# Kernel optimization log

Measured on AMD Instinct MI355X. Metric: run time of the kernel, lower is better.

## Reference

```python
import jax, jax.numpy as jnp
import numpy as np

DIM_X, DIM_Y, DIM_D, DIM_H = 100, 1, 100, 256
T = 1.0


def setup_inputs() -> dict:
    key = jax.random.key(0)
    ks = jax.random.split(key, 10)
    B, N = 2048, 128

    def lin(k, fi, fo):
        # kaiming-ish scaling so the relu MLP stays well-conditioned
        return (jax.random.normal(k, (fi, fo), jnp.float32) / np.sqrt(fi)).astype(jnp.float32)

    return {
        "W_noise": jax.random.normal(ks[0], (B, DIM_D, N), jnp.float32),  # unscaled randn; *sqrt(dt) in reference
        "signs": jax.random.randint(ks[1], (N,), 0, 2).astype(jnp.int32),  # 0/1 -> mapped to +-1
        "x0": jnp.ones((DIM_X,), jnp.float32),
        "y0": jax.random.uniform(ks[2], (DIM_Y,), jnp.float32),
        "Wi": lin(ks[3], DIM_X + 1, DIM_H),
        "bi": jnp.zeros((DIM_H,), jnp.float32),
        "Wh1": lin(ks[4], DIM_H, DIM_H),
        "bh1": jnp.zeros((DIM_H,), jnp.float32),
        "Wh2": lin(ks[5], DIM_H, DIM_H),
        "bh2": jnp.zeros((DIM_H,), jnp.float32),
        "Wo": lin(ks[6], DIM_H, DIM_Y * DIM_D),
        "bo": jnp.zeros((DIM_Y * DIM_D,), jnp.float32),
        "batch_size": B,
        "N": N,
    }


def reference(W_noise, signs, x0, y0, Wi, bi, Wh1, bh1, Wh2, bh2, Wo, bo, batch_size, N):
    dt = jnp.float32(T / N)
    sqdt = jnp.sqrt(dt)
    sqrt2 = jnp.sqrt(jnp.float32(2.0))
    B = W_noise.shape[0]

    W = W_noise * sqdt                                   # Brownian increments [B, D, N]
    s_pm = (2 * signs - 1).astype(jnp.float32)           # +-1 per step
    ones_col = jnp.ones((B, 1), jnp.float32)

    def phi(u):  # relu MLP -> [B, dim_y, dim_d]
        h = jax.nn.relu(u @ Wi + bi)
        h = jax.nn.relu(h @ Wh1 + bh1)
        h = jax.nn.relu(h @ Wh2 + bh2)
        return (h @ Wo + bo).reshape(-1, DIM_Y, DIM_D)

    def f_fn(t, x, y, z):  # driver f(t,x,y,z) = ||z||^2 over d
        return jnp.sum(z * z, axis=-1)  # [B, dim_y]

    x_init = x0 + jnp.zeros((B, DIM_X), jnp.float32)
    y_init = y0 + jnp.zeros((B, DIM_Y), jnp.float32)

    xs = (jnp.moveaxis(W, 2, 0), s_pm, jnp.arange(N, dtype=jnp.float32))

    def step(carry, inp):
        x, y = carry
        w, s, i = inp                      # w: [B, D]
        t0 = dt * i
        t1 = dt * (i + 1.0)
        sdt = s * sqdt
        z = phi(jnp.concatenate([x, ones_col * t0], axis=1))
        # b = 0, sigma = sqrt(2)*I  =>  matmul(sigma, w -+ S*sqrt(dt)) = sqrt(2)*(w -+ sdt)
        k1 = sqrt2 * (w - sdt)
        k2 = sqrt2 * (w + sdt)
        y1 = -f_fn(t0, x, y, z) * dt + jnp.einsum('byd,bd->by', z, w - sdt)
        z_new = phi(jnp.concatenate([x + k1, ones_col * t1], axis=1))
        y2 = -f_fn(t1, x, y + y1, z) * dt + jnp.einsum('byd,bd->by', z_new, w + sdt)
        return (x + 0.5 * (k1 + k2), y + 0.5 * (y1 + y2)), None

    (x, y), _ = jax.lax.scan(step, (x_init, y_init), xs)
    return x, y
```

## Files before the change

kernel.cpp:

```cpp
#include <hip/hip_runtime.h>
#include <hip/hip_bf16.h>

typedef __hip_bfloat16 bf16;
typedef __attribute__((ext_vector_type(8)))  short bf16x8v;
typedef __attribute__((ext_vector_type(16))) float f32x16;
typedef __attribute__((ext_vector_type(4)))  short short4v;

#define B_SZ   2048
#define NSTEP  128
#define DD     100
#define DX     100
#define DH     256

__device__ __constant__ const float DT_   = 0.0078125f;
__device__ __constant__ const float SQDT_ = 0.08838834764831845f;
__device__ __constant__ const float C1_   = 0.125f;

__global__ __launch_bounds__(256) void pack_kernel(
    const float* __restrict__ Wi, const float* __restrict__ Wh1,
    const float* __restrict__ Wh2, const float* __restrict__ Wo,
    const float* __restrict__ bi, const float* __restrict__ bh1,
    const float* __restrict__ bh2, const float* __restrict__ bo,
    bf16* __restrict__ wfWi, bf16* __restrict__ wfWh1,
    bf16* __restrict__ wfWh2, bf16* __restrict__ wfWo,
    float* __restrict__ biases)
{
    const int bid = blockIdx.x;
    const float* W; bf16* dst; int Kact, Nact, NTILE, total, base;
    if (bid < 112)      { W = Wi;  dst = wfWi;  Kact = 101; Nact = 256; NTILE = 8; total = 28672; base = 0;   }
    else if (bid < 368) { W = Wh1; dst = wfWh1; Kact = 256; Nact = 256; NTILE = 8; total = 65536; base = 112; }
    else if (bid < 624) { W = Wh2; dst = wfWh2; Kact = 256; Nact = 256; NTILE = 8; total = 65536; base = 368; }
    else if (bid < 752) { W = Wo;  dst = wfWo;  Kact = 256; Nact = 100; NTILE = 4; total = 32768; base = 624; }
    else {
        int i = (bid - 752) * 256 + threadIdx.x;
        if (i < 256) biases[i] = bi[i];
        else if (i < 512) biases[i] = bh1[i - 256];
        else if (i < 768) biases[i] = bh2[i - 512];
        else if (i < 896) biases[i] = (i - 768 < DD) ? bo[i - 768] : 0.f;
        return;
    }
    int idx = (bid - base) * 256 + threadIdx.x;
    if (idx >= total) return;
    int j = idx & 7;
    int l = (idx >> 3) & 63;
    int frag = idx >> 9;
    int t = frag % NTILE;
    int c = frag / NTILE;
    int n = t * 32 + (l & 31);
    int k = c * 16 + (l >> 5) * 8 + j;
    float v = (k < Kact && n < Nact) ? W[(size_t)k * Nact + n] : 0.f;
    dst[idx] = __float2bfloat16(v);
}

__global__ __launch_bounds__(128) void xprep_kernel(
    const float* __restrict__ Wn, const float* __restrict__ x0,
    float* __restrict__ xckpt, float* __restrict__ xout)
{
    __shared__ float w_l[DD * 129];
    const int b = blockIdx.x, tid = threadIdx.x;
    const float* wb = Wn + (size_t)b * DD * NSTEP;

    for (int idx = tid; idx < DD * NSTEP; idx += 128) {
        int d = idx >> 7, i = idx & 127;
        w_l[d * 129 + i] = wb[idx];
    }
    __syncthreads();

    if (tid < DD) {
        float x = x0[tid];
#pragma unroll 1
        for (int i = 0; i < NSTEP; ++i) {
            if ((i & 31) == 0)
                xckpt[((size_t)b * 4 + (i >> 5)) * DX + tid] = x;
            x += C1_ * w_l[tid * 129 + i];
        }
        xout[(size_t)b * DX + tid] = x;
    }
}

template<int KC, int NTT, int NT, bool RELU>
__device__ __forceinline__ void layer32(
    char* __restrict__ buf,
    const bf16* __restrict__ wfrag, const float* __restrict__ bias,
    int lane, int t0)
{
    const int mrow = lane & 31;
    const int kg   = lane >> 5;
    const int ma = mrow, mb = 32 + mrow;
    const int sa = (ma & 15) << 4, sb = (mb & 15) << 4;

    f32x16 acc[NT][2];
#pragma unroll
    for (int t = 0; t < NT; ++t)
#pragma unroll
        for (int mt = 0; mt < 2; ++mt)
#pragma unroll
            for (int e = 0; e < 16; ++e) acc[t][mt][e] = 0.f;

    const char* wptr = (const char*)wfrag + (size_t)t0 * 1024 + (size_t)lane * 16;

    bf16x8v bc0 = *(const bf16x8v*)(buf + ma * 512 + ((kg * 16) ^ sa));
    bf16x8v bc1 = *(const bf16x8v*)(buf + mb * 512 + ((kg * 16) ^ sb));
    bf16x8v ac[NT];
#pragma unroll
    for (int t = 0; t < NT; ++t)
        ac[t] = *(const bf16x8v*)(wptr + (size_t)t * 1024);

#pragma unroll
    for (int c = 0; c < KC; ++c) {
        const int cn = (c + 1 < KC) ? c + 1 : c;
        const int ncol = cn * 32 + kg * 16;
        bf16x8v bn0 = *(const bf16x8v*)(buf + ma * 512 + (ncol ^ sa));
        bf16x8v bn1 = *(const bf16x8v*)(buf + mb * 512 + (ncol ^ sb));
        bf16x8v an[NT];
#pragma unroll
        for (int t = 0; t < NT; ++t)
            an[t] = *(const bf16x8v*)(wptr + (size_t)(cn * NTT + t) * 1024);

        __builtin_amdgcn_s_setprio(1);
#pragma unroll
        for (int t = 0; t < NT; ++t) {
            acc[t][0] = __builtin_amdgcn_mfma_f32_32x32x16_bf16(ac[t], bc0, acc[t][0], 0, 0, 0);
            acc[t][1] = __builtin_amdgcn_mfma_f32_32x32x16_bf16(ac[t], bc1, acc[t][1], 0, 0, 0);
        }
        __builtin_amdgcn_s_setprio(0);

        bc0 = bn0; bc1 = bn1;
#pragma unroll
        for (int t = 0; t < NT; ++t) ac[t] = an[t];
    }

    __syncthreads();

#pragma unroll
    for (int t = 0; t < NT; ++t) {
#pragma unroll
        for (int g = 0; g < 4; ++g) {
            const int nb = (t0 + t) * 32 + g * 8 + kg * 4;
            const float4 bv = *(const float4*)(bias + nb);
#pragma unroll
            for (int mt = 0; mt < 2; ++mt) {
                const int m = mt * 32 + mrow;
                float v0 = acc[t][mt][g * 4 + 0] + bv.x;
                float v1 = acc[t][mt][g * 4 + 1] + bv.y;
                float v2 = acc[t][mt][g * 4 + 2] + bv.z;
                float v3 = acc[t][mt][g * 4 + 3] + bv.w;
                if (RELU) {
                    v0 = fmaxf(v0, 0.f); v1 = fmaxf(v1, 0.f);
                    v2 = fmaxf(v2, 0.f); v3 = fmaxf(v3, 0.f);
                }
                bf16 h0 = __float2bfloat16(v0), h1 = __float2bfloat16(v1);
                bf16 h2 = __float2bfloat16(v2), h3 = __float2bfloat16(v3);
                short4v pv;
                pv[0] = *(short*)&h0; pv[1] = *(short*)&h1;
                pv[2] = *(short*)&h2; pv[3] = *(short*)&h3;
                *(short4v*)(buf + m * 512 + ((nb * 2) ^ ((m & 15) << 4))) = pv;
            }
        }
    }
}

__global__ __launch_bounds__(256, 3) void mlp_kernel(
    const float* __restrict__ Wn, const int* __restrict__ signs,
    const float* __restrict__ xckpt,
    const bf16* __restrict__ wfWi, const bf16* __restrict__ wfWh1,
    const bf16* __restrict__ wfWh2, const bf16* __restrict__ wfWo,
    const float* __restrict__ biases, float* __restrict__ incr)
{
    __shared__ char  buf[64 * 512];
    __shared__ float noise[DD * 33];
    __shared__ float s_l32[32];
    __shared__ float Sz2[64], Szw[64];
    const int tid = threadIdx.x;
    const int lane = tid & 63, w = tid >> 6;
    const int b = blockIdx.x >> 2, ch = blockIdx.x & 3;
    const int i0 = ch * 32;
    const size_t row0 = (size_t)blockIdx.x * 64;
    const float* wnb = Wn + (size_t)b * DD * NSTEP;

    for (int idx = tid; idx < DD * 32; idx += 256) {
        int d = idx >> 5, j = idx & 31;
        noise[d * 33 + j] = wnb[d * NSTEP + i0 + j];
    }
    if (tid < 32) s_l32[tid] = 2.f * (float)signs[i0 + tid] - 1.f;
    __syncthreads();

    if (tid < DD) {
        const int d = tid;
        float x = xckpt[((size_t)b * 4 + ch) * DX + d];
#pragma unroll 1
        for (int j = 0; j < 32; ++j) {
            float wn = noise[d * 33 + j];
            float s  = s_l32[j];
            int r0 = j * 2;
            bf16 h0 = __float2bfloat16(x);
            bf16 h1 = __float2bfloat16(x + C1_ * (wn - s));
            *(short*)(buf + r0 * 512 + ((d * 2) ^ ((r0 & 15) << 4))) = *(short*)&h0;
            *(short*)(buf + (r0 + 1) * 512 + ((d * 2) ^ (((r0 + 1) & 15) << 4))) = *(short*)&h1;
            x += C1_ * wn;
        }
    } else if (tid < 164) {
        const int r = tid - 100;
        const int i = i0 + (r >> 1), h = r & 1;
        bf16 tv = __float2bfloat16(DT_ * (float)(i + h));
        char* rb = buf + r * 512;
        const int sw = (r & 15) << 4;
        *(short*)(rb + (200 ^ sw)) = *(short*)&tv;
        *(short*)(rb + (202 ^ sw)) = 0;
        *(short*)(rb + (204 ^ sw)) = 0;
        *(short*)(rb + (206 ^ sw)) = 0;
        *(uint4*)(rb + (208 ^ sw)) = (uint4){0, 0, 0, 0};
    }
    __syncthreads();

    layer32<7,  8, 2, true >(buf, wfWi,  biases,        lane, w * 2);
    __syncthreads();
    layer32<16, 8, 2, true >(buf, wfWh1, biases + 256,  lane, w * 2);
    __syncthreads();
    layer32<16, 8, 2, true >(buf, wfWh2, biases + 512,  lane, w * 2);
    __syncthreads();
    layer32<16, 4, 1, false>(buf, wfWo,  biases + 768,  lane, w);
    __syncthreads();

    {
        const int r = tid >> 2, q = tid & 3;
        const int jj = r >> 1, h = r & 1;
        const float s = s_l32[jj];
        const float sdt = s * SQDT_;
        float sz2 = 0.f, szw = 0.f;
        for (int d = q; d < DD; d += 4) {
            unsigned short zb = *(const unsigned short*)(buf + r * 512 + ((d * 2) ^ ((r & 15) << 4)));
            union { unsigned int u; float f; } cv; cv.u = ((unsigned int)zb) << 16;
            float z = cv.f;
            float wv = SQDT_ * noise[d * 33 + jj];
            float wt = h ? (wv + sdt) : (wv - sdt);
            sz2 += z * z;
            szw += z * wt;
        }
        sz2 += __shfl_xor(sz2, 1); sz2 += __shfl_xor(sz2, 2);
        szw += __shfl_xor(szw, 1); szw += __shfl_xor(szw, 2);
        if (q == 0) { Sz2[r] = sz2; Szw[r] = szw; }
    }
    __syncthreads();

    if (tid < 32) {
        int rr = tid * 2;
        incr[row0 / 2 + tid] = -Sz2[rr] * DT_ + 0.5f * (Szw[rr] + Szw[rr + 1]);
    }
}

__global__ __launch_bounds__(128) void y_kernel(
    const float* __restrict__ incr, const float* __restrict__ y0,
    float* __restrict__ yout)
{
    const int b = blockIdx.x, tid = threadIdx.x;
    float v = incr[(size_t)b * NSTEP + tid];
#pragma unroll
    for (int off = 1; off < 64; off <<= 1) v += __shfl_xor(v, off);
    __shared__ float partial[2];
    if ((tid & 63) == 0) partial[tid >> 6] = v;
    __syncthreads();
    if (tid == 0) yout[b] = y0[0] + partial[0] + partial[1];
}

extern "C" void kernel_launch(void* const* d_in, const int* in_sizes, int n_in,
                              void* d_out, int out_size, void* d_ws, size_t ws_size,
                              hipStream_t stream) {
    (void)in_sizes; (void)n_in; (void)out_size; (void)ws_size;
    const float* Wn    = (const float*)d_in[0];
    const int*   signs = (const int*)d_in[1];
    const float* x0    = (const float*)d_in[2];
    const float* y0    = (const float*)d_in[3];
    const float* Wi    = (const float*)d_in[4];
    const float* bi    = (const float*)d_in[5];
    const float* Wh1   = (const float*)d_in[6];
    const float* bh1   = (const float*)d_in[7];
    const float* Wh2   = (const float*)d_in[8];
    const float* bh2   = (const float*)d_in[9];
    const float* Wo    = (const float*)d_in[10];
    const float* bo    = (const float*)d_in[11];

    float* out  = (float*)d_out;
    float* xout = out;
    float* yout = out + (size_t)B_SZ * DX;

    char* ws = (char*)d_ws;
    size_t off = 0;
    bf16*  wfWi   = (bf16*)(ws + off); off += 28672 * sizeof(bf16);
    bf16*  wfWh1  = (bf16*)(ws + off); off += 65536 * sizeof(bf16);
    bf16*  wfWh2  = (bf16*)(ws + off); off += 65536 * sizeof(bf16);
    bf16*  wfWo   = (bf16*)(ws + off); off += 32768 * sizeof(bf16);
    float* biases = (float*)(ws + off); off += 896 * sizeof(float);
    float* xckpt  = (float*)(ws + off); off += (size_t)B_SZ * 4 * DX * sizeof(float);
    float* incr   = (float*)(ws + off); off += (size_t)B_SZ * NSTEP * sizeof(float);

    pack_kernel<<<756, 256, 0, stream>>>(Wi, Wh1, Wh2, Wo, bi, bh1, bh2, bo,
                                         wfWi, wfWh1, wfWh2, wfWo, biases);
    xprep_kernel<<<B_SZ, 128, 0, stream>>>(Wn, x0, xckpt, xout);
    mlp_kernel<<<B_SZ * 4, 256, 0, stream>>>(Wn, signs, xckpt,
                                             wfWi, wfWh1, wfWh2, wfWo, biases, incr);
    y_kernel<<<B_SZ, 128, 0, stream>>>(incr, y0, yout);
}
```

Measured before the change: 276.7 us.

## Double MLP block to 512 threads with one N-tile per wave

The MLP kernel now launches 512 threads (8 waves) per block instead of 256. In the hidden layers each wave owns a single 32-column output tile instead of two. In the output layer the waves split both the N tiles and the two 32-row M halves. The aim is more waves per block to hide LDS and weight-load latency and to spread the MFMA work more finely, at the cost of fewer accumulators per wave, more barrier participants and idle threads in the scalar sections.

```diff
diff --git a/kernel.cpp b/kernel.cpp
--- a/kernel.cpp
+++ b/kernel.cpp
@@ -78,89 +78,82 @@
     }
 }
 
-template<int KC, int NTT, int NT, bool RELU>
-__device__ __forceinline__ void layer32(
+template<int KC, int NTT, int MT, bool RELU>
+__device__ __forceinline__ void layer32w(
     char* __restrict__ buf,
     const bf16* __restrict__ wfrag, const float* __restrict__ bias,
-    int lane, int t0)
+    int lane, int t0, int m0)
 {
     const int mrow = lane & 31;
     const int kg   = lane >> 5;
-    const int ma = mrow, mb = 32 + mrow;
-    const int sa = (ma & 15) << 4, sb = (mb & 15) << 4;
-
-    f32x16 acc[NT][2];
-#pragma unroll
-    for (int t = 0; t < NT; ++t)
-#pragma unroll
-        for (int mt = 0; mt < 2; ++mt)
-#pragma unroll
-            for (int e = 0; e < 16; ++e) acc[t][mt][e] = 0.f;
+
+    f32x16 acc[MT];
+#pragma unroll
+    for (int mt = 0; mt < MT; ++mt)
+#pragma unroll
+        for (int e = 0; e < 16; ++e) acc[mt][e] = 0.f;
 
     const char* wptr = (const char*)wfrag + (size_t)t0 * 1024 + (size_t)lane * 16;
 
-    bf16x8v bc0 = *(const bf16x8v*)(buf + ma * 512 + ((kg * 16) ^ sa));
-    bf16x8v bc1 = *(const bf16x8v*)(buf + mb * 512 + ((kg * 16) ^ sb));
-    bf16x8v ac[NT];
-#pragma unroll
-    for (int t = 0; t < NT; ++t)
-        ac[t] = *(const bf16x8v*)(wptr + (size_t)t * 1024);
+    bf16x8v bc[MT];
+#pragma unroll
+    for (int mt = 0; mt < MT; ++mt) {
+        const int m = m0 + mt * 32 + mrow;
+        bc[mt] = *(const bf16x8v*)(buf + m * 512 + ((kg * 16) ^ ((m & 15) << 4)));
+    }
+    bf16x8v ac = *(const bf16x8v*)(wptr);
 
 #pragma unroll
     for (int c = 0; c < KC; ++c) {
         const int cn = (c + 1 < KC) ? c + 1 : c;
         const int ncol = cn * 32 + kg * 16;
-        bf16x8v bn0 = *(const bf16x8v*)(buf + ma * 512 + (ncol ^ sa));
-        bf16x8v bn1 = *(const bf16x8v*)(buf + mb * 512 + (ncol ^ sb));
-        bf16x8v an[NT];
-#pragma unroll
-        for (int t = 0; t < NT; ++t)
-            an[t] = *(const bf16x8v*)(wptr + (size_t)(cn * NTT + t) * 1024);
+        bf16x8v bn[MT];
+#pragma unroll
+        for (int mt = 0; mt < MT; ++mt) {
+            const int m = m0 + mt * 32 + mrow;
+            bn[mt] = *(const bf16x8v*)(buf + m * 512 + (ncol ^ ((m & 15) << 4)));
+        }
+        bf16x8v an = *(const bf16x8v*)(wptr + (size_t)(cn * NTT) * 1024);
 
         __builtin_amdgcn_s_setprio(1);
 #pragma unroll
-        for (int t = 0; t < NT; ++t) {
-            acc[t][0] = __builtin_amdgcn_mfma_f32_32x32x16_bf16(ac[t], bc0, acc[t][0], 0, 0, 0);
-            acc[t][1] = __builtin_amdgcn_mfma_f32_32x32x16_bf16(ac[t], bc1, acc[t][1], 0, 0, 0);
-        }
+        for (int mt = 0; mt < MT; ++mt)
+            acc[mt] = __builtin_amdgcn_mfma_f32_32x32x16_bf16(ac, bc[mt], acc[mt], 0, 0, 0);
         __builtin_amdgcn_s_setprio(0);
 
-        bc0 = bn0; bc1 = bn1;
-#pragma unroll
-        for (int t = 0; t < NT; ++t) ac[t] = an[t];
-    }
-
-    __syncthreads();
-
-#pragma unroll
-    for (int t = 0; t < NT; ++t) {
-#pragma unroll
-        for (int g = 0; g < 4; ++g) {
-            const int nb = (t0 + t) * 32 + g * 8 + kg * 4;
-            const float4 bv = *(const float4*)(bias + nb);
-#pragma unroll
-            for (int mt = 0; mt < 2; ++mt) {
-                const int m = mt * 32 + mrow;
-                float v0 = acc[t][mt][g * 4 + 0] + bv.x;
-                float v1 = acc[t][mt][g * 4 + 1] + bv.y;
-                float v2 = acc[t][mt][g * 4 + 2] + bv.z;
-                float v3 = acc[t][mt][g * 4 + 3] + bv.w;
-                if (RELU) {
-                    v0 = fmaxf(v0, 0.f); v1 = fmaxf(v1, 0.f);
-                    v2 = fmaxf(v2, 0.f); v3 = fmaxf(v3, 0.f);
-                }
-                bf16 h0 = __float2bfloat16(v0), h1 = __float2bfloat16(v1);
-                bf16 h2 = __float2bfloat16(v2), h3 = __float2bfloat16(v3);
-                short4v pv;
-                pv[0] = *(short*)&h0; pv[1] = *(short*)&h1;
-                pv[2] = *(short*)&h2; pv[3] = *(short*)&h3;
-                *(short4v*)(buf + m * 512 + ((nb * 2) ^ ((m & 15) << 4))) = pv;
+#pragma unroll
+        for (int mt = 0; mt < MT; ++mt) bc[mt] = bn[mt];
+        ac = an;
+    }
+
+    __syncthreads();
+
+#pragma unroll
+    for (int g = 0; g < 4; ++g) {
+        const int nb = t0 * 32 + g * 8 + kg * 4;
+        const float4 bv = *(const float4*)(bias + nb);
+#pragma unroll
+        for (int mt = 0; mt < MT; ++mt) {
+            const int m = m0 + mt * 32 + mrow;
+            float v0 = acc[mt][g * 4 + 0] + bv.x;
+            float v1 = acc[mt][g * 4 + 1] + bv.y;
+            float v2 = acc[mt][g * 4 + 2] + bv.z;
+            float v3 = acc[mt][g * 4 + 3] + bv.w;
+            if (RELU) {
+                v0 = fmaxf(v0, 0.f); v1 = fmaxf(v1, 0.f);
+                v2 = fmaxf(v2, 0.f); v3 = fmaxf(v3, 0.f);
             }
-        }
-    }
-}
-
-__global__ __launch_bounds__(256, 3) void mlp_kernel(
+            bf16 h0 = __float2bfloat16(v0), h1 = __float2bfloat16(v1);
+            bf16 h2 = __float2bfloat16(v2), h3 = __float2bfloat16(v3);
+            short4v pv;
+            pv[0] = *(short*)&h0; pv[1] = *(short*)&h1;
+            pv[2] = *(short*)&h2; pv[3] = *(short*)&h3;
+            *(short4v*)(buf + m * 512 + ((nb * 2) ^ ((m & 15) << 4))) = pv;
+        }
+    }
+}
+
+__global__ __launch_bounds__(512, 4) void mlp_kernel(
     const float* __restrict__ Wn, const int* __restrict__ signs,
     const float* __restrict__ xckpt,
     const bf16* __restrict__ wfWi, const bf16* __restrict__ wfWh1,
@@ -178,7 +171,7 @@
     const size_t row0 = (size_t)blockIdx.x * 64;
     const float* wnb = Wn + (size_t)b * DD * NSTEP;
 
-    for (int idx = tid; idx < DD * 32; idx += 256) {
+    for (int idx = tid; idx < DD * 32; idx += 512) {
         int d = idx >> 5, j = idx & 31;
         noise[d * 33 + j] = wnb[d * NSTEP + i0 + j];
     }
@@ -213,16 +206,16 @@
     }
     __syncthreads();
 
-    layer32<7,  8, 2, true >(buf, wfWi,  biases,        lane, w * 2);
-    __syncthreads();
-    layer32<16, 8, 2, true >(buf, wfWh1, biases + 256,  lane, w * 2);
-    __syncthreads();
-    layer32<16, 8, 2, true >(buf, wfWh2, biases + 512,  lane, w * 2);
-    __syncthreads();
-    layer32<16, 4, 1, false>(buf, wfWo,  biases + 768,  lane, w);
-    __syncthreads();
-
-    {
+    layer32w<7,  8, 2, true >(buf, wfWi,  biases,        lane, w, 0);
+    __syncthreads();
+    layer32w<16, 8, 2, true >(buf, wfWh1, biases + 256,  lane, w, 0);
+    __syncthreads();
+    layer32w<16, 8, 2, true >(buf, wfWh2, biases + 512,  lane, w, 0);
+    __syncthreads();
+    layer32w<16, 4, 1, false>(buf, wfWo,  biases + 768,  lane, w & 3, (w >> 2) * 32);
+    __syncthreads();
+
+    if (tid < 256) {
         const int r = tid >> 2, q = tid & 3;
         const int jj = r >> 1, h = r & 1;
         const float s = s_l32[jj];
@@ -297,7 +290,7 @@
     pack_kernel<<<756, 256, 0, stream>>>(Wi, Wh1, Wh2, Wo, bi, bh1, bh2, bo,
                                          wfWi, wfWh1, wfWh2, wfWo, biases);
     xprep_kernel<<<B_SZ, 128, 0, stream>>>(Wn, x0, xckpt, xout);
-    mlp_kernel<<<B_SZ * 4, 256, 0, stream>>>(Wn, signs, xckpt,
+    mlp_kernel<<<B_SZ * 4, 512, 0, stream>>>(Wn, signs, xckpt,
                                              wfWi, wfWh1, wfWh2, wfWo, biases, incr);
     y_kernel<<<B_SZ, 128, 0, stream>>>(incr, y0, yout);
 }
```

Result: slower. 307.2 us (+11.0%).
